# Optimization experiments

Measured on AMD Instinct MI355X. Metric: run time of the kernel, lower is better.

Reference implementation:

```python
import jax, jax.numpy as jnp
import numpy as np

LP, LQ, B, D0, H = 128, 128, 64, 150, 150
D = 2 * D0  # in_size after self-concatenation


def setup_inputs() -> dict:
    key = jax.random.key(0)
    ks = jax.random.split(key, 12)
    s = 0.08  # weight scale to keep tanh/sigmoid out of hard saturation
    return {
        "Up": jax.random.normal(ks[0], (LP, B, D0), jnp.float32),
        "Uq": jax.random.normal(ks[1], (LQ, B, D0), jnp.float32),
        "Wp": jax.random.normal(ks[2], (H, D), jnp.float32) * s,
        "Wq": jax.random.normal(ks[3], (H, D), jnp.float32) * s,
        "Wv": jax.random.normal(ks[4], (H, H), jnp.float32) * s,
        "Wg": jax.random.normal(ks[5], (2 * D, 2 * D), jnp.float32) * s,
        "V": jax.random.normal(ks[6], (B, H), jnp.float32) * s,
        "v0": jax.random.normal(ks[7], (B, H), jnp.float32) * s,
        "W_ih": jax.random.normal(ks[8], (3 * H, 2 * D), jnp.float32) * s,
        "W_hh": jax.random.normal(ks[9], (3 * H, H), jnp.float32) * s,
        "b_ih": jax.random.normal(ks[10], (3 * H,), jnp.float32) * s,
        "b_hh": jax.random.normal(ks[11], (3 * H,), jnp.float32) * s,
    }


def reference(Up, Uq, Wp, Wq, Wv, Wg, V, v0, W_ih, W_hh, b_ih, b_hh):
    # self-concat of features, as in the original forward
    Upc = jnp.concatenate([Up, Up], axis=2)  # (LP, B, D)
    Uqc = jnp.concatenate([Uq, Uq], axis=2)  # (LQ, B, D)
    # Wq @ Uq is loop-invariant in the original; hoist it (same math)
    Wuq = jnp.einsum('lbd,hd->lbh', Uqc, Wq)  # (LQ, B, H)

    def step(v, up_i):
        # up_i: (B, D); v: (B, H)
        wup = up_i @ Wp.T                                   # (B, H)
        x = jnp.tanh(wup[None] + Wuq + (v @ Wv.T)[None])    # (LQ, B, H)
        s = jnp.einsum('lbh,bh->bl', x, V)                  # (B, LQ)
        a = jax.nn.softmax(s, axis=1)
        c = jnp.einsum('bl,lbd->bd', a, Uqc)                # (B, D)
        r = jnp.concatenate([up_i, c], axis=1)              # (B, 2D)
        r = jax.nn.sigmoid(r @ Wg.T) * r                    # gated input
        # PyTorch GRUCell math
        gi = r @ W_ih.T + b_ih                              # (B, 3H)
        gh = v @ W_hh.T + b_hh                              # (B, 3H)
        i_r, i_z, i_n = jnp.split(gi, 3, axis=1)
        h_r, h_z, h_n = jnp.split(gh, 3, axis=1)
        rr = jax.nn.sigmoid(i_r + h_r)
        zz = jax.nn.sigmoid(i_z + h_z)
        n = jnp.tanh(i_n + rr * h_n)
        h = (1.0 - zz) * n + zz * v
        return h, h

    _, vs = jax.lax.scan(step, v0, Upc)  # vs: (LP, B, H)
    return vs  # dropout in eval mode = identity
```

## Files before the change

kernel.cpp:

```cpp
#include <hip/hip_runtime.h>
#include <hip/hip_fp16.h>

typedef _Float16 h2_t __attribute__((ext_vector_type(2)));

__device__ __forceinline__ float dot2f(int w, int x, float acc) {
#if __has_builtin(__builtin_amdgcn_fdot2)
  return __builtin_amdgcn_fdot2(__builtin_bit_cast(h2_t, w),
                                __builtin_bit_cast(h2_t, x), acc, false);
#else
  h2_t a = __builtin_bit_cast(h2_t, w);
  h2_t b = __builtin_bit_cast(h2_t, x);
  return acc + (float)a[0] * (float)b[0] + (float)a[1] * (float)b[1];
#endif
}

__device__ __forceinline__ float rcp_f(float x) {
#if __has_builtin(__builtin_amdgcn_rcpf)
  return __builtin_amdgcn_rcpf(x);
#else
  return 1.0f / x;
#endif
}

__device__ __forceinline__ float fast_tanh(float x) {
  float e = exp2f(x * 2.885390082f);
  return 1.0f - 2.0f * rcp_f(e + 1.0f);
}
__device__ __forceinline__ float fast_sigmoid(float x) {
  return rcp_f(1.0f + exp2f(x * -1.442695041f));
}
__device__ __forceinline__ int packh2(float a, float b) {
  h2_t h;
  h[0] = (_Float16)a;
  h[1] = (_Float16)b;
  return __builtin_bit_cast(int, h);
}

__device__ __forceinline__ int ldi_coh(const int* p) {
  return __hip_atomic_load((int*)p, __ATOMIC_RELAXED, __HIP_MEMORY_SCOPE_AGENT);
}
__device__ __forceinline__ float ldf_coh(const float* p) {
  return __hip_atomic_load((float*)p, __ATOMIC_RELAXED,
                           __HIP_MEMORY_SCOPE_AGENT);
}
__device__ __forceinline__ void sti_coh(int* p, int v) {
  __hip_atomic_store(p, v, __ATOMIC_RELAXED, __HIP_MEMORY_SCOPE_AGENT);
}
__device__ __forceinline__ void stf_coh(float* p, float v) {
  __hip_atomic_store(p, v, __ATOMIC_RELAXED, __HIP_MEMORY_SCOPE_AGENT);
}

#define DOTC(W, X, A)                                                          \
  {                                                                            \
    int4 _x = (X);                                                             \
    A = dot2f((W).x, _x.x, A);                                                 \
    A = dot2f((W).y, _x.y, A);                                                 \
    A = dot2f((W).z, _x.z, A);                                                 \
    A = dot2f((W).w, _x.w, A);                                                 \
  }

__global__ void prep_weights(const float* __restrict__ Wp,
                             const float* __restrict__ Wv,
                             const float* __restrict__ Wg,
                             const float* __restrict__ Wih,
                             const float* __restrict__ Whh,
                             __half* __restrict__ oMa, __half* __restrict__ oWg,
                             __half* __restrict__ oWih,
                             __half* __restrict__ oWhh, int* __restrict__ flags,
                             int* __restrict__ payload) {
  if (blockIdx.x == 0) {
    for (int j = threadIdx.x; j < 1024; j += 256) flags[j] = 0;
  }
  if (blockIdx.x == 1 && threadIdx.x < 128) {
    int cc = threadIdx.x >> 1, s = threadIdx.x & 1;
    payload[cc * 4096 + 150 + s] = 0;
  }
  int idx = blockIdx.x * 256 + threadIdx.x;
  const int NMa = 150 * 304, NWg = 600 * 304, NWih = 900 * 304,
            NWhh = 452 * 152;
  if (idx < NMa) {
    int r = idx / 304, c = idx % 304;
    float v = 0.f;
    if (c < 150)
      v = Wp[r * 300 + c] + Wp[r * 300 + 150 + c];
    else if (c >= 152 && c < 302)
      v = Wv[r * 150 + (c - 152)];
    oMa[(c >> 3) * 1200 + r * 8 + (c & 7)] = __float2half(v);
    return;
  }
  idx -= NMa;
  if (idx < NWg) {
    int r = idx / 304, c = idx % 304;
    float v = 0.f;
    if (c < 150)
      v = Wg[r * 600 + c] + Wg[r * 600 + 150 + c];
    else if (c >= 152 && c < 302) {
      int d = c - 152;
      v = Wg[r * 600 + 300 + d] + Wg[r * 600 + 450 + d];
    }
    oWg[(c >> 3) * 4800 + r * 8 + (c & 7)] = __float2half(v);
    return;
  }
  idx -= NWg;
  if (idx < NWih) {
    int s = idx / 304, c = idx % 304;
    int r = s >> 1, off = (s & 1) * 300;
    float v = (c < 300) ? Wih[r * 600 + off + c] : 0.f;
    oWih[(c >> 3) * 7200 + s * 8 + (c & 7)] = __float2half(v);
    return;
  }
  idx -= NWih;
  if (idx < NWhh) {
    int r = idx / 152, c = idx % 152;
    float v = (r < 450 && c < 150) ? Whh[r * 150 + c] : 0.f;
    oWhh[(c >> 3) * 3616 + r * 8 + (c & 7)] = __float2half(v);
  }
}

__global__ __launch_bounds__(256) void prep_wuq(const float* __restrict__ Uq,
                                                const float* __restrict__ Wq,
                                                __half* __restrict__ oWuq,
                                                __half* __restrict__ oUqh) {
  __shared__ float sUql[64 * 150];
  const int l = blockIdx.x, tid = threadIdx.x;
  for (int idx = tid; idx < 9600; idx += 256) sUql[idx] = Uq[l * 9600 + idx];
  __syncthreads();
  for (int idx = tid; idx < 64 * 152; idx += 256) {
    int bb = idx / 152, d = idx % 152;
    float v = (d < 150) ? sUql[bb * 150 + d] : 0.f;
    oUqh[(size_t)bb * 19456 + l * 152 + d] = __float2half(v);
  }
  if (tid < 152) {
    const int h = tid;
    if (h < 150) {
      float wq[150];
#pragma unroll
      for (int d = 0; d < 150; ++d)
        wq[d] = Wq[h * 300 + d] + Wq[h * 300 + 150 + d];
      for (int bb = 0; bb < 64; ++bb) {
        float acc = 0.f;
#pragma unroll
        for (int d = 0; d < 150; ++d) acc += wq[d] * sUql[bb * 150 + d];
        oWuq[(size_t)bb * 19456 + l * 152 + h] = __float2half(acc);
      }
    } else {
      for (int bb = 0; bb < 64; ++bb)
        oWuq[(size_t)bb * 19456 + l * 152 + h] = __float2half(0.f);
    }
  }
}

__device__ __forceinline__ void post_and_wait(int* f4, int q, int target) {
  __syncthreads();
  if (threadIdx.x == 0) sti_coh(&f4[q], target);
  if (threadIdx.x < 4) {
    int spins = 0;
    while (ldi_coh(&f4[threadIdx.x]) < target && ++spins < (1 << 20)) {
    }
  }
  __syncthreads();
}

__global__ __launch_bounds__(1024, 1) void pq_main(
    const float* __restrict__ Up, const float* __restrict__ V,
    const float* __restrict__ v0, const float* __restrict__ b_ih,
    const float* __restrict__ b_hh, const int* __restrict__ gWuq,
    const __half* __restrict__ gUqh, const int* __restrict__ gMa,
    const int* __restrict__ gWg, const int* __restrict__ gWih,
    const int* __restrict__ gWhh, int* __restrict__ flags,
    int* __restrict__ payload, float* __restrict__ out) {
  __shared__ __align__(16) float sTV[304];
  __shared__ __align__(16) float sV[152];
  __shared__ __align__(16) float sGh[456];
  __shared__ __align__(16) float sS[128];
  __shared__ __align__(16) float sC0[152];
  __shared__ __align__(16) float sCp[608];
  __shared__ __align__(16) float sU[152];
  __shared__ __align__(16) float sv_[152];
  __shared__ __align__(16) int sXd[152];
  __shared__ __align__(16) int svh[76];
  __shared__ __align__(16) int sRgh[304];
  __shared__ __align__(16) float sGi[456];
  __shared__ __align__(16) float sBih[456];
  __shared__ __align__(16) float sBhh[456];
  extern __shared__ __align__(16) int dynlds[];
  int* sWuq = dynlds;
  __half* sUqh = (__half*)(dynlds + 9728);

  const int t = threadIdx.x;
  const int c = blockIdx.x & 63;
  const int q = blockIdx.x >> 6;
  const int b = c;

  int* myflags = flags + c * 16;
  int* pl = payload + c * 4096;
  float* plT = (float*)pl;
  float* plGh = (float*)(pl + 160);
  float* plGi = (float*)(pl + 640);

  const int4* MaT4 = (const int4*)gMa;
  const int4* WgT4 = (const int4*)gWg;
  const int4* WihT4 = (const int4*)gWih;
  const int4* WhhT4 = (const int4*)gWhh;

  const int baseR = 113 * q - (q == 3 ? 1 : 0);
  const int cntR = (q < 2) ? 113 : 112;
  const int c_lo = (q == 0) ? 0 : (q == 1) ? 18 : (q == 2) ? 38 : 56;
  const int c_hi = (q == 0) ? 18 : (q == 1) ? 37 : (q == 2) ? 56 : 75;

  int4 a0, a1, a2, a3, a4, a5, a6, a7, a8, a9;
  int4 b0, b1, b2, b3, b4, b5, b6, b7, b8, b9;
  {
    const int4* p;
    int nr, sub, step, nch, row;
    if (t < 152) {
      p = MaT4; nr = 150; step = 4; nch = 38;
      sub = t & 3; row = 38 * q + (t >> 2);
      if (row > 149) row = 149;
    } else if (t < 378) {
      p = WhhT4; nr = 452; step = 2; nch = 19;
      int u2 = t - 152; sub = u2 & 1; row = baseR + (u2 >> 1);
    } else if (t >= 384 && t < 984) {
      p = WgT4; nr = 600; step = 4; nch = 38;
      int u2 = t - 384; sub = u2 & 3; row = 150 * q + (u2 >> 2);
    } else {
      p = MaT4; nr = 150; step = 4; nch = 38; sub = 0; row = 0;
    }
#define LDA(i)                                                                 \
  {                                                                            \
    int cc = sub + step * (i);                                                 \
    if (cc > nch - 1) cc = nch - 1;                                            \
    a##i = p[cc * nr + row];                                                   \
  }
    LDA(0) LDA(1) LDA(2) LDA(3) LDA(4) LDA(5) LDA(6) LDA(7) LDA(8) LDA(9)
#undef LDA
  }
  {
    int row = (t < 900) ? (t >> 1) : 0;
    int sub = (t < 900) ? (t & 1) : 0;
#define LDB(i)                                                                 \
  {                                                                            \
    int cq = c_lo + sub + 2 * (i);                                             \
    if (cq > c_hi) cq = c_hi;                                                  \
    int hf = (cq >= 38) ? 1 : 0;                                               \
    int cc = cq - 38 * hf;                                                     \
    b##i = WihT4[cc * 900 + 2 * row + hf];                                     \
  }
    LDB(0) LDB(1) LDB(2) LDB(3) LDB(4) LDB(5) LDB(6) LDB(7) LDB(8) LDB(9)
#undef LDB
  }

  for (int idx = t; idx < 9728; idx += 1024) sWuq[idx] = gWuq[b * 9728 + idx];
  {
    const int* gU2 = (const int*)(gUqh + (size_t)b * 19456);
    int* sU2 = (int*)sUqh;
    for (int idx = t; idx < 9728; idx += 1024) sU2[idx] = gU2[idx];
  }
  if (t < 150) {
    sV[t] = V[b * 150 + t];
    float v_ = v0[b * 150 + t];
    sv_[t] = v_;
    float vn = __shfl_down(v_, 1);
    if (!(t & 1)) svh[t >> 1] = packh2(v_, vn);
    float u_ = Up[b * 150 + t];
    sU[t] = u_;
    float un = __shfl_down(u_, 1);
    if (!(t & 1)) sXd[t >> 1] = packh2(u_, un);
  }
  for (int idx = t; idx < 450; idx += 1024) {
    sBih[idx] = b_ih[idx];
    sBhh[idx] = b_hh[idx];
  }
  if (t < 304) sRgh[t] = 0;
  if (t == 0) {
    svh[75] = 0;
    sXd[75] = 0;
    sXd[151] = 0;
    sV[150] = 0.f;
    sV[151] = 0.f;
  }
  const int4* sXd4 = (const int4*)sXd;
  const int4* svh4 = (const int4*)svh;
  const int4* sRgh4 = (const int4*)sRgh;
  const int c_lq = t / 150;
  const int c_d0 = t - c_lq * 150;
  __syncthreads();

#pragma unroll 1
  for (int i = 0; i < 128; ++i) {
    float unext = 0.f;
    if (t >= 640 && t < 790) {
      int ii = (i < 127) ? (i + 1) : 127;
      unext = Up[ii * 9600 + b * 150 + (t - 640)];
    }

    if (t < 152) {
      int rl = t >> 2, sub = t & 3;
      int h = 38 * q + rl;
      float acc = 0.f;
#define MAD(i2)                                                                \
  {                                                                            \
    int cc = sub + 4 * (i2);                                                   \
    if (cc < 38) {                                                             \
      int4 x = (cc < 19) ? sXd4[cc] : svh4[cc - 19];                           \
      DOTC(a##i2, x, acc)                                                      \
    }                                                                          \
  }
      MAD(0) MAD(1) MAD(2) MAD(3) MAD(4) MAD(5) MAD(6) MAD(7) MAD(8) MAD(9)
#undef MAD
      acc += __shfl_xor(acc, 1);
      acc += __shfl_xor(acc, 2);
      if (sub == 0 && h < 150) stf_coh(&plT[h], acc);
    } else if (t < 378) {
      int u2 = t - 152;
      int rl = u2 >> 1, sub = u2 & 1;
      int r = baseR + rl;
      float acc = 0.f;
#define HHD(i2)                                                                \
  {                                                                            \
    int cc = sub + 2 * (i2);                                                   \
    if (cc < 19) DOTC(a##i2, svh4[cc], acc)                                    \
  }
      HHD(0) HHD(1) HHD(2) HHD(3) HHD(4) HHD(5) HHD(6) HHD(7) HHD(8) HHD(9)
#undef HHD
      acc += __shfl_xor(acc, 1);
      if (sub == 0 && rl < cntR) stf_coh(&plGh[r], acc + sBhh[r]);
    }
    post_and_wait(myflags, q, i + 1);
    if (t < 76) {
      float x0 = ldf_coh(&plT[2 * t]);
      float x1 = ldf_coh(&plT[2 * t + 1]);
      float4 tv;
      tv.x = x0;
      tv.y = x1;
      tv.z = sV[2 * t];
      tv.w = sV[2 * t + 1];
      ((float4*)sTV)[t] = tv;
    } else if (t >= 128 && t < 578) {
      sGh[t - 128] = ldf_coh(&plGh[t - 128]);
    }
    __syncthreads();

    {
      const int l = t >> 3, sub = t & 7;
      const int base = l * 76;
      const int niter = (sub < 3) ? 10 : 9;
      float acc = 0.f;
#pragma unroll
      for (int k = 0; k < 10; ++k) {
        if (k < niter) {
          int w = sub + 8 * k;
          int qq = sWuq[base + w];
          float4 tv = ((const float4*)sTV)[w];
          h2_t hq = __builtin_bit_cast(h2_t, qq);
          float x0 = (float)hq[0] + tv.x;
          float x1 = (float)hq[1] + tv.y;
          acc += fast_tanh(x0) * tv.z;
          acc += fast_tanh(x1) * tv.w;
        }
      }
      acc += __shfl_xor(acc, 1);
      acc += __shfl_xor(acc, 2);
      acc += __shfl_xor(acc, 4);
      if (sub == 0) sS[l] = acc;
    }
    __syncthreads();

    if (t < 64) {
      float s0 = sS[t], s1 = sS[t + 64];
      float m = fmaxf(s0, s1);
#pragma unroll
      for (int o = 1; o < 64; o <<= 1) m = fmaxf(m, __shfl_xor(m, o));
      float e0 = exp2f((s0 - m) * 1.442695041f);
      float e1 = exp2f((s1 - m) * 1.442695041f);
      float sum = e0 + e1;
#pragma unroll
      for (int o = 1; o < 64; o <<= 1) sum += __shfl_xor(sum, o);
      float inv = rcp_f(sum);
      sS[t] = e0 * inv;
      sS[t + 64] = e1 * inv;
    }
    __syncthreads();

    if (t < 600) {
      const __half* src = sUqh + c_lq * 32 * 152 + c_d0;
      float acc = 0.f;
#pragma unroll
      for (int j = 0; j < 32; ++j) {
        float a = sS[c_lq * 32 + j];
        acc += a * __half2float(src[j * 152]);
      }
      sCp[c_lq * 152 + c_d0] = acc;
    }
    __syncthreads();
    if (t < 150) {
      float c0 = sCp[t] + sCp[152 + t] + sCp[304 + t] + sCp[456 + t];
      sC0[t] = c0;
      float cn = __shfl_down(c0, 1);
      if (!(t & 1)) sXd[76 + (t >> 1)] = packh2(c0, cn);
    }
    __syncthreads();

    if (t >= 384 && t < 984) {
      int u2 = t - 384;
      int rl = u2 >> 2, sub = u2 & 3;
      int j = 150 * q + rl;
      float acc = 0.f;
#define WGD(i2)                                                                \
  {                                                                            \
    int cc = sub + 4 * (i2);                                                   \
    if (cc < 38) DOTC(a##i2, sXd4[cc], acc)                                    \
  }
      WGD(0) WGD(1) WGD(2) WGD(3) WGD(4) WGD(5) WGD(6) WGD(7) WGD(8) WGD(9)
#undef WGD
      acc += __shfl_xor(acc, 1);
      acc += __shfl_xor(acc, 2);
      if (sub == 0) {
        float rb;
        if (j < 150)
          rb = sU[j];
        else if (j < 300)
          rb = sU[j - 150];
        else if (j < 450)
          rb = sC0[j - 300];
        else
          rb = sC0[j - 450];
        float rg = rb * fast_sigmoid(acc);
        ((__half*)sRgh)[(j < 300) ? j : (j + 4)] = __float2half(rg);
      }
    }
    __syncthreads();

    if (t < 900) {
      int row = t >> 1, sub = t & 1;
      float acc = 0.f;
#define IHD(i2)                                                                \
  {                                                                            \
    int cq = c_lo + sub + 2 * (i2);                                            \
    if (cq <= c_hi) DOTC(b##i2, sRgh4[cq], acc)                                \
  }
      IHD(0) IHD(1) IHD(2) IHD(3) IHD(4) IHD(5) IHD(6) IHD(7) IHD(8) IHD(9)
#undef IHD
      acc += __shfl_xor(acc, 1);
      if (!sub) stf_coh(&plGi[456 * q + row], acc);
    }
    post_and_wait(myflags + 4, q, i + 1);
    if (t < 450) {
      float g0 = ldf_coh(&plGi[t]);
      float g1 = ldf_coh(&plGi[456 + t]);
      float g2 = ldf_coh(&plGi[912 + t]);
      float g3 = ldf_coh(&plGi[1368 + t]);
      sGi[t] = g0 + g1 + g2 + g3 + sBih[t];
    }
    __syncthreads();

    if (t < 150) {
      float ir = sGi[t], iz = sGi[150 + t], in_ = sGi[300 + t];
      float hr = sGh[t], hz = sGh[150 + t], hn = sGh[300 + t];
      float rr = fast_sigmoid(ir + hr);
      float zz = fast_sigmoid(iz + hz);
      float nn = fast_tanh(in_ + rr * hn);
      float vold = sv_[t];
      float hv = nn + zz * (vold - nn);
      if (q == 0) out[i * 9600 + b * 150 + t] = hv;
      sv_[t] = hv;
      float hv1 = __shfl_down(hv, 1);
      if (!(t & 1)) svh[t >> 1] = packh2(hv, hv1);
    } else if (t >= 640 && t < 790) {
      int t2 = t - 640;
      sU[t2] = unext;
      float un = __shfl_down(unext, 1);
      if (!(t2 & 1)) sXd[t2 >> 1] = packh2(unext, un);
    }
    __syncthreads();
  }
}

extern "C" void kernel_launch(void* const* d_in, const int* in_sizes, int n_in,
                              void* d_out, int out_size, void* d_ws,
                              size_t ws_size, hipStream_t stream) {
  const float* Up = (const float*)d_in[0];
  const float* Uq = (const float*)d_in[1];
  const float* Wp = (const float*)d_in[2];
  const float* Wq = (const float*)d_in[3];
  const float* Wv = (const float*)d_in[4];
  const float* Wg = (const float*)d_in[5];
  const float* V = (const float*)d_in[6];
  const float* v0 = (const float*)d_in[7];
  const float* Wih = (const float*)d_in[8];
  const float* Whh = (const float*)d_in[9];
  const float* bih = (const float*)d_in[10];
  const float* bhh = (const float*)d_in[11];

  char* ws = (char*)d_ws;
  __half* wsWuq = (__half*)(ws);
  __half* wsUqh = (__half*)(ws + 2490368);
  __half* wsMa = (__half*)(ws + 4980736);
  __half* wsWg = (__half*)(ws + 5071936);
  __half* wsWih = (__half*)(ws + 5436736);
  __half* wsWhh = (__half*)(ws + 5983936);
  int* wsFlags = (int*)(ws + 6121472);
  int* wsPayload = (int*)(ws + 6125568);

  (void)hipFuncSetAttribute((const void*)pq_main,
                            hipFuncAttributeMaxDynamicSharedMemorySize, 77824);

  prep_weights<<<2228, 256, 0, stream>>>(Wp, Wv, Wg, Wih, Whh, wsMa, wsWg,
                                         wsWih, wsWhh, wsFlags, wsPayload);
  prep_wuq<<<128, 256, 0, stream>>>(Uq, Wq, wsWuq, wsUqh);
  pq_main<<<256, 1024, 77824, stream>>>(Up, V, v0, bih, bhh, (const int*)wsWuq,
                                        wsUqh, (const int*)wsMa,
                                        (const int*)wsWg, (const int*)wsWih,
                                        (const int*)wsWhh, wsFlags, wsPayload,
                                        (float*)d_out);
}
```

Baseline: 1.439 ms.

## Drop a GRU barrier, double-buffer gh payload, split accumulators in dot loops

The GRU gate stage now reads the cross-block gi partials and the gh values straight from the coherent payload, instead of staging them in shared memory behind an extra __syncthreads. The gh payload is double-buffered by step parity, so the next step's writes cannot overwrite values still being read. The context reduction is split across twice as many partial slots using packed half2 loads. All the dot-product loops use two independent accumulators to shorten dependency chains. The cost is more global coherent loads per gate thread and an 8-way sum for the context vector.

```diff
diff --git a/kernel.cpp b/kernel.cpp
--- a/kernel.cpp
+++ b/kernel.cpp
@@ -171,16 +171,14 @@
     int* __restrict__ payload, float* __restrict__ out) {
   __shared__ __align__(16) float sTV[304];
   __shared__ __align__(16) float sV[152];
-  __shared__ __align__(16) float sGh[456];
   __shared__ __align__(16) float sS[128];
   __shared__ __align__(16) float sC0[152];
-  __shared__ __align__(16) float sCp[608];
+  __shared__ __align__(16) float sCp[1216];
   __shared__ __align__(16) float sU[152];
   __shared__ __align__(16) float sv_[152];
   __shared__ __align__(16) int sXd[152];
   __shared__ __align__(16) int svh[76];
   __shared__ __align__(16) int sRgh[304];
-  __shared__ __align__(16) float sGi[456];
   __shared__ __align__(16) float sBih[456];
   __shared__ __align__(16) float sBhh[456];
   extern __shared__ __align__(16) int dynlds[];
@@ -195,8 +193,9 @@
   int* myflags = flags + c * 16;
   int* pl = payload + c * 4096;
   float* plT = (float*)pl;
-  float* plGh = (float*)(pl + 160);
-  float* plGi = (float*)(pl + 640);
+  float* plGh0 = (float*)(pl + 160);
+  float* plGh1 = (float*)(pl + 672);
+  float* plGi = (float*)(pl + 1184);
 
   const int4* MaT4 = (const int4*)gMa;
   const int4* WgT4 = (const int4*)gWg;
@@ -282,12 +281,11 @@
   const int4* sXd4 = (const int4*)sXd;
   const int4* svh4 = (const int4*)svh;
   const int4* sRgh4 = (const int4*)sRgh;
-  const int c_lq = t / 150;
-  const int c_d0 = t - c_lq * 150;
   __syncthreads();
 
 #pragma unroll 1
   for (int i = 0; i < 128; ++i) {
+    float* plGhW = (i & 1) ? plGh1 : plGh0;
     float unext = 0.f;
     if (t >= 640 && t < 790) {
       int ii = (i < 127) ? (i + 1) : 127;
@@ -297,17 +295,19 @@
     if (t < 152) {
       int rl = t >> 2, sub = t & 3;
       int h = 38 * q + rl;
-      float acc = 0.f;
-#define MAD(i2)                                                                \
+      float acc0 = 0.f, acc1 = 0.f;
+#define MAD(i2, A)                                                             \
   {                                                                            \
     int cc = sub + 4 * (i2);                                                   \
     if (cc < 38) {                                                             \
       int4 x = (cc < 19) ? sXd4[cc] : svh4[cc - 19];                           \
-      DOTC(a##i2, x, acc)                                                      \
+      DOTC(a##i2, x, A)                                                        \
     }                                                                          \
   }
-      MAD(0) MAD(1) MAD(2) MAD(3) MAD(4) MAD(5) MAD(6) MAD(7) MAD(8) MAD(9)
+      MAD(0, acc0) MAD(1, acc1) MAD(2, acc0) MAD(3, acc1) MAD(4, acc0)
+      MAD(5, acc1) MAD(6, acc0) MAD(7, acc1) MAD(8, acc0) MAD(9, acc1)
 #undef MAD
+      float acc = acc0 + acc1;
       acc += __shfl_xor(acc, 1);
       acc += __shfl_xor(acc, 2);
       if (sub == 0 && h < 150) stf_coh(&plT[h], acc);
@@ -315,16 +315,18 @@
       int u2 = t - 152;
       int rl = u2 >> 1, sub = u2 & 1;
       int r = baseR + rl;
-      float acc = 0.f;
-#define HHD(i2)                                                                \
+      float acc0 = 0.f, acc1 = 0.f;
+#define HHD(i2, A)                                                             \
   {                                                                            \
     int cc = sub + 2 * (i2);                                                   \
-    if (cc < 19) DOTC(a##i2, svh4[cc], acc)                                    \
-  }
-      HHD(0) HHD(1) HHD(2) HHD(3) HHD(4) HHD(5) HHD(6) HHD(7) HHD(8) HHD(9)
+    if (cc < 19) DOTC(a##i2, svh4[cc], A)                                      \
+  }
+      HHD(0, acc0) HHD(1, acc1) HHD(2, acc0) HHD(3, acc1) HHD(4, acc0)
+      HHD(5, acc1) HHD(6, acc0) HHD(7, acc1) HHD(8, acc0) HHD(9, acc1)
 #undef HHD
+      float acc = acc0 + acc1;
       acc += __shfl_xor(acc, 1);
-      if (sub == 0 && rl < cntR) stf_coh(&plGh[r], acc + sBhh[r]);
+      if (sub == 0 && rl < cntR) stf_coh(&plGhW[r], acc + sBhh[r]);
     }
     post_and_wait(myflags, q, i + 1);
     if (t < 76) {
@@ -336,8 +338,6 @@
       tv.z = sV[2 * t];
       tv.w = sV[2 * t + 1];
       ((float4*)sTV)[t] = tv;
-    } else if (t >= 128 && t < 578) {
-      sGh[t - 128] = ldf_coh(&plGh[t - 128]);
     }
     __syncthreads();
 
@@ -383,18 +383,31 @@
     __syncthreads();
 
     if (t < 600) {
-      const __half* src = sUqh + c_lq * 32 * 152 + c_d0;
-      float acc = 0.f;
-#pragma unroll
-      for (int j = 0; j < 32; ++j) {
-        float a = sS[c_lq * 32 + j];
-        acc += a * __half2float(src[j * 152]);
+      const int lq = t / 150, rem = t - lq * 150;
+      const int d2 = rem >> 1, jh = rem & 1;
+      const int lbase = lq * 32 + jh * 16;
+      const int* srcI = (const int*)sUqh;
+      const int abase = lbase;
+      int addr = lbase * 76 + d2;
+      float p0 = 0.f, p1 = 0.f;
+#pragma unroll
+      for (int j = 0; j < 16; ++j) {
+        float a = sS[abase + j];
+        h2_t hp = __builtin_bit_cast(h2_t, srcI[addr + j * 76]);
+        p0 += a * (float)hp[0];
+        p1 += a * (float)hp[1];
       }
-      sCp[c_lq * 152 + c_d0] = acc;
+      float2 pr;
+      pr.x = p0;
+      pr.y = p1;
+      ((float2*)sCp)[(jh * 608 + lq * 152) / 2 + d2] = pr;
     }
     __syncthreads();
     if (t < 150) {
-      float c0 = sCp[t] + sCp[152 + t] + sCp[304 + t] + sCp[456 + t];
+      float c0 = 0.f;
+#pragma unroll
+      for (int s8 = 0; s8 < 8; ++s8)
+        c0 += sCp[(s8 & 1) * 608 + (s8 >> 1) * 152 + t];
       sC0[t] = c0;
       float cn = __shfl_down(c0, 1);
       if (!(t & 1)) sXd[76 + (t >> 1)] = packh2(c0, cn);
@@ -405,14 +418,16 @@
       int u2 = t - 384;
       int rl = u2 >> 2, sub = u2 & 3;
       int j = 150 * q + rl;
-      float acc = 0.f;
-#define WGD(i2)                                                                \
+      float acc0 = 0.f, acc1 = 0.f;
+#define WGD(i2, A)                                                             \
   {                                                                            \
     int cc = sub + 4 * (i2);                                                   \
-    if (cc < 38) DOTC(a##i2, sXd4[cc], acc)                                    \
-  }
-      WGD(0) WGD(1) WGD(2) WGD(3) WGD(4) WGD(5) WGD(6) WGD(7) WGD(8) WGD(9)
+    if (cc < 38) DOTC(a##i2, sXd4[cc], A)                                      \
+  }
+      WGD(0, acc0) WGD(1, acc1) WGD(2, acc0) WGD(3, acc1) WGD(4, acc0)
+      WGD(5, acc1) WGD(6, acc0) WGD(7, acc1) WGD(8, acc0) WGD(9, acc1)
 #undef WGD
+      float acc = acc0 + acc1;
       acc += __shfl_xor(acc, 1);
       acc += __shfl_xor(acc, 2);
       if (sub == 0) {
@@ -433,30 +448,32 @@
 
     if (t < 900) {
       int row = t >> 1, sub = t & 1;
-      float acc = 0.f;
-#define IHD(i2)                                                                \
+      float acc0 = 0.f, acc1 = 0.f;
+#define IHD(i2, A)                                                             \
   {                                                                            \
     int cq = c_lo + sub + 2 * (i2);                                            \
-    if (cq <= c_hi) DOTC(b##i2, sRgh4[cq], acc)                                \
-  }
-      IHD(0) IHD(1) IHD(2) IHD(3) IHD(4) IHD(5) IHD(6) IHD(7) IHD(8) IHD(9)
+    if (cq <= c_hi) DOTC(b##i2, sRgh4[cq], A)                                  \
+  }
+      IHD(0, acc0) IHD(1, acc1) IHD(2, acc0) IHD(3, acc1) IHD(4, acc0)
+      IHD(5, acc1) IHD(6, acc0) IHD(7, acc1) IHD(8, acc0) IHD(9, acc1)
 #undef IHD
+      float acc = acc0 + acc1;
       acc += __shfl_xor(acc, 1);
       if (!sub) stf_coh(&plGi[456 * q + row], acc);
     }
     post_and_wait(myflags + 4, q, i + 1);
-    if (t < 450) {
-      float g0 = ldf_coh(&plGi[t]);
-      float g1 = ldf_coh(&plGi[456 + t]);
-      float g2 = ldf_coh(&plGi[912 + t]);
-      float g3 = ldf_coh(&plGi[1368 + t]);
-      sGi[t] = g0 + g1 + g2 + g3 + sBih[t];
-    }
-    __syncthreads();
 
     if (t < 150) {
-      float ir = sGi[t], iz = sGi[150 + t], in_ = sGi[300 + t];
-      float hr = sGh[t], hz = sGh[150 + t], hn = sGh[300 + t];
+      float ir = sBih[t], iz = sBih[150 + t], in_ = sBih[300 + t];
+#pragma unroll
+      for (int qq = 0; qq < 4; ++qq) {
+        ir += ldf_coh(&plGi[456 * qq + t]);
+        iz += ldf_coh(&plGi[456 * qq + 150 + t]);
+        in_ += ldf_coh(&plGi[456 * qq + 300 + t]);
+      }
+      float hr = ldf_coh(&plGhW[t]);
+      float hz = ldf_coh(&plGhW[150 + t]);
+      float hn = ldf_coh(&plGhW[300 + t]);
       float rr = fast_sigmoid(ir + hr);
       float zz = fast_sigmoid(iz + hz);
       float nn = fast_tanh(in_ + rr * hn);
```

Measured after the change: 1.751 ms. 1.22x slower.

## Split dot accumulators and precompute Wg up-half during idle pre-barrier phase

Applied to the files above, without the earlier changes.

Each register-resident dot product now alternates between two accumulators, which breaks the serial fdot2 dependency chain and adds ILP. Threads 384-983 were idle during the first phase, so they now compute the part of the Wg gate product that depends only on the Up half (chunks below 19) before the cross-block barrier. After the context vector is ready they finish only the remaining chunks. This takes work off the critical path after the attention step, at the cost of extra live registers across barriers and a changed summation order.

```diff
diff --git a/kernel.cpp b/kernel.cpp
--- a/kernel.cpp
+++ b/kernel.cpp
@@ -288,6 +288,7 @@
 
 #pragma unroll 1
   for (int i = 0; i < 128; ++i) {
+    float accD0 = 0.f, accD1 = 0.f;
     float unext = 0.f;
     if (t >= 640 && t < 790) {
       int ii = (i < 127) ? (i + 1) : 127;
@@ -297,17 +298,19 @@
     if (t < 152) {
       int rl = t >> 2, sub = t & 3;
       int h = 38 * q + rl;
-      float acc = 0.f;
-#define MAD(i2)                                                                \
+      float acc0 = 0.f, acc1 = 0.f;
+#define MAD(i2, A)                                                             \
   {                                                                            \
     int cc = sub + 4 * (i2);                                                   \
     if (cc < 38) {                                                             \
       int4 x = (cc < 19) ? sXd4[cc] : svh4[cc - 19];                           \
-      DOTC(a##i2, x, acc)                                                      \
+      DOTC(a##i2, x, A)                                                        \
     }                                                                          \
   }
-      MAD(0) MAD(1) MAD(2) MAD(3) MAD(4) MAD(5) MAD(6) MAD(7) MAD(8) MAD(9)
+      MAD(0, acc0) MAD(1, acc1) MAD(2, acc0) MAD(3, acc1) MAD(4, acc0)
+      MAD(5, acc1) MAD(6, acc0) MAD(7, acc1) MAD(8, acc0) MAD(9, acc1)
 #undef MAD
+      float acc = acc0 + acc1;
       acc += __shfl_xor(acc, 1);
       acc += __shfl_xor(acc, 2);
       if (sub == 0 && h < 150) stf_coh(&plT[h], acc);
@@ -315,16 +318,27 @@
       int u2 = t - 152;
       int rl = u2 >> 1, sub = u2 & 1;
       int r = baseR + rl;
-      float acc = 0.f;
-#define HHD(i2)                                                                \
+      float acc0 = 0.f, acc1 = 0.f;
+#define HHD(i2, A)                                                             \
   {                                                                            \
     int cc = sub + 2 * (i2);                                                   \
-    if (cc < 19) DOTC(a##i2, svh4[cc], acc)                                    \
-  }
-      HHD(0) HHD(1) HHD(2) HHD(3) HHD(4) HHD(5) HHD(6) HHD(7) HHD(8) HHD(9)
+    if (cc < 19) DOTC(a##i2, svh4[cc], A)                                      \
+  }
+      HHD(0, acc0) HHD(1, acc1) HHD(2, acc0) HHD(3, acc1) HHD(4, acc0)
+      HHD(5, acc1) HHD(6, acc0) HHD(7, acc1) HHD(8, acc0) HHD(9, acc1)
 #undef HHD
+      float acc = acc0 + acc1;
       acc += __shfl_xor(acc, 1);
       if (sub == 0 && rl < cntR) stf_coh(&plGh[r], acc + sBhh[r]);
+    } else if (t >= 384 && t < 984) {
+      int sub = (t - 384) & 3;
+#define WGU(i2, A)                                                             \
+  {                                                                            \
+    int cc = sub + 4 * (i2);                                                   \
+    if (cc < 19) DOTC(a##i2, sXd4[cc], A)                                      \
+  }
+      WGU(0, accD0) WGU(1, accD1) WGU(2, accD0) WGU(3, accD1) WGU(4, accD0)
+#undef WGU
     }
     post_and_wait(myflags, q, i + 1);
     if (t < 76) {
@@ -405,14 +419,15 @@
       int u2 = t - 384;
       int rl = u2 >> 2, sub = u2 & 3;
       int j = 150 * q + rl;
-      float acc = 0.f;
-#define WGD(i2)                                                                \
+#define WGC(i2, A)                                                             \
   {                                                                            \
     int cc = sub + 4 * (i2);                                                   \
-    if (cc < 38) DOTC(a##i2, sXd4[cc], acc)                                    \
-  }
-      WGD(0) WGD(1) WGD(2) WGD(3) WGD(4) WGD(5) WGD(6) WGD(7) WGD(8) WGD(9)
-#undef WGD
+    if (cc >= 19 && cc < 38) DOTC(a##i2, sXd4[cc], A)                          \
+  }
+      WGC(4, accD1) WGC(5, accD0) WGC(6, accD1) WGC(7, accD0) WGC(8, accD1)
+      WGC(9, accD0)
+#undef WGC
+      float acc = accD0 + accD1;
       acc += __shfl_xor(acc, 1);
       acc += __shfl_xor(acc, 2);
       if (sub == 0) {
@@ -433,14 +448,16 @@
 
     if (t < 900) {
       int row = t >> 1, sub = t & 1;
-      float acc = 0.f;
-#define IHD(i2)                                                                \
+      float acc0 = 0.f, acc1 = 0.f;
+#define IHD(i2, A)                                                             \
   {                                                                            \
     int cq = c_lo + sub + 2 * (i2);                                            \
-    if (cq <= c_hi) DOTC(b##i2, sRgh4[cq], acc)                                \
-  }
-      IHD(0) IHD(1) IHD(2) IHD(3) IHD(4) IHD(5) IHD(6) IHD(7) IHD(8) IHD(9)
+    if (cq <= c_hi) DOTC(b##i2, sRgh4[cq], A)                                  \
+  }
+      IHD(0, acc0) IHD(1, acc1) IHD(2, acc0) IHD(3, acc1) IHD(4, acc0)
+      IHD(5, acc1) IHD(6, acc0) IHD(7, acc1) IHD(8, acc0) IHD(9, acc1)
 #undef IHD
+      float acc = acc0 + acc1;
       acc += __shfl_xor(acc, 1);
       if (!sub) stf_coh(&plGi[456 * q + row], acc);
     }
```

Measured after the change: 1.441 ms. No clear change (+0.2%).
